# Optimization experiments

Measured on AMD Instinct MI355X. Metric: run time of the kernel, lower is better.

Reference implementation:

```python
import jax, jax.numpy as jnp
import numpy as np

SPIKE_COUNT = 3   # init kwarg spike_count
DT = 0.001        # init kwarg dt; convert_indices_to_times=True


def setup_inputs() -> dict:
    key = jax.random.key(0)
    T, B, N = 512, 64, 2048
    spike_input = jax.random.bernoulli(key, 0.05, (T, B, N)).astype(jnp.float32)
    return {"spike_input": spike_input}


def reference(spike_input):
    """Return times of the first SPIKE_COUNT spikes along the time axis for
    each (batch, output) channel, ascending; channels with fewer spikes are
    padded with inf. Matches norse ToSpikeTimes followed by * dt.
    Input: [T, B, N] -> output: [SPIKE_COUNT, B, N]."""
    T = spike_input.shape[0]
    t_idx = jnp.arange(T, dtype=spike_input.dtype)[:, None, None]        # [T,1,1]
    masked = jnp.where(spike_input > 0, t_idx, jnp.inf)                  # [T,B,N]
    # smallest SPIKE_COUNT indices per channel via top_k on the negation
    neg = -jnp.moveaxis(masked, 0, -1)                                   # [B,N,T]
    vals, _ = jax.lax.top_k(neg, SPIKE_COUNT)                            # [B,N,k]
    spike_idx = jnp.moveaxis(-vals, -1, 0)                               # [k,B,N], ascending
    return spike_idx * DT
```

## Files before the change

kernel.cpp:

```cpp
#include <hip/hip_runtime.h>
#include <cmath>


constexpr int K_SPIKES = 3;
constexpr int CHUNK = 16;

__global__ __launch_bounds__(256) void spikes_to_times_kernel(
    const float* __restrict__ in, float* __restrict__ out,
    int BN, int T, float dt) {
  const int c = blockIdx.x * blockDim.x + threadIdx.x;
  if (c >= BN) return;

  float t0 = INFINITY, t1 = INFINITY, t2 = INFINITY;
  int cnt = 0;
  const float* p = in + c;

  for (int t = 0; t < T; t += CHUNK) {
    float v[CHUNK];
#pragma unroll
    for (int j = 0; j < CHUNK; ++j) {
      v[j] = p[(size_t)(t + j) * (size_t)BN];
    }
#pragma unroll
    for (int j = 0; j < CHUNK; ++j) {
      const bool s = v[j] > 0.0f;
      const float tt = (float)(t + j);
      if (s && cnt == 0) t0 = tt;
      if (s && cnt == 1) t1 = tt;
      if (s && cnt == 2) t2 = tt;
      cnt += s ? 1 : 0;
    }
    if (__all(cnt >= K_SPIKES)) break;
  }

  out[c]          = t0 * dt;
  out[BN + c]     = t1 * dt;
  out[2 * BN + c] = t2 * dt;
}

extern "C" void kernel_launch(void* const* d_in, const int* in_sizes, int n_in,
                              void* d_out, int out_size, void* d_ws, size_t ws_size,
                              hipStream_t stream) {
  const float* in = (const float*)d_in[0];
  float* out = (float*)d_out;

  const int BN = out_size / K_SPIKES;
  const int T = in_sizes[0] / BN;

  const int block = 256;
  const int grid = (BN + block - 1) / block;
  hipLaunchKernelGGL(spikes_to_times_kernel, dim3(grid), dim3(block), 0, stream,
                     in, out, BN, T, 0.001f);
}
```

Measured before the change: 26.99 us.

## Software-pipeline chunk loads with four rotating register buffers

Result: slower. 35.45 us (+31.3%).

```diff
diff --git a/kernel.cpp b/kernel.cpp
--- a/kernel.cpp
+++ b/kernel.cpp
@@ -11,27 +11,61 @@
   const int c = blockIdx.x * blockDim.x + threadIdx.x;
   if (c >= BN) return;
 
+  const int nchunks = (T + CHUNK - 1) / CHUNK;
+  const float* p = in + c;
+
   float t0 = INFINITY, t1 = INFINITY, t2 = INFINITY;
   int cnt = 0;
-  const float* p = in + c;
 
-  for (int t = 0; t < T; t += CHUNK) {
-    float v[CHUNK];
-#pragma unroll
-    for (int j = 0; j < CHUNK; ++j) {
-      v[j] = p[(size_t)(t + j) * (size_t)BN];
-    }
-#pragma unroll
-    for (int j = 0; j < CHUNK; ++j) {
-      const bool s = v[j] > 0.0f;
-      const float tt = (float)(t + j);
-      if (s && cnt == 0) t0 = tt;
-      if (s && cnt == 1) t1 = tt;
-      if (s && cnt == 2) t2 = tt;
-      cnt += s ? 1 : 0;
-    }
+  float b0[CHUNK], b1[CHUNK], b2[CHUNK], b3[CHUNK];
+
+#define LOADC(dst, ci)                                                   \
+  do {                                                                   \
+    const int cc_ = ((ci) < nchunks) ? (ci) : (nchunks - 1);             \
+    _Pragma("unroll") for (int j = 0; j < CHUNK; ++j) {                  \
+      dst[j] = p[(size_t)(cc_ * CHUNK + j) * (size_t)BN];                \
+    }                                                                    \
+  } while (0)
+
+#define PROC(src, ci)                                                    \
+  do {                                                                   \
+    if ((ci) < nchunks) {                                                \
+      _Pragma("unroll") for (int j = 0; j < CHUNK; ++j) {                \
+        const int ti_ = (ci) * CHUNK + j;                                \
+        const bool s_ = (src[j] > 0.0f) && (ti_ < T);                    \
+        const float tt_ = (float)ti_;                                    \
+        if (s_ && cnt == 0) t0 = tt_;                                    \
+        if (s_ && cnt == 1) t1 = tt_;                                    \
+        if (s_ && cnt == 2) t2 = tt_;                                    \
+        cnt += s_ ? 1 : 0;                                               \
+      }                                                                  \
+    }                                                                    \
+  } while (0)
+
+  LOADC(b0, 0);
+  LOADC(b1, 1);
+  LOADC(b2, 2);
+
+  for (int base = 0; base < nchunks; base += 4) {
+    LOADC(b3, base + 3);
+    PROC(b0, base + 0);
+    if (__all(cnt >= K_SPIKES)) break;
+
+    LOADC(b0, base + 4);
+    PROC(b1, base + 1);
+    if (__all(cnt >= K_SPIKES)) break;
+
+    LOADC(b1, base + 5);
+    PROC(b2, base + 2);
+    if (__all(cnt >= K_SPIKES)) break;
+
+    LOADC(b2, base + 6);
+    PROC(b3, base + 3);
     if (__all(cnt >= K_SPIKES)) break;
   }
+
+#undef LOADC
+#undef PROC
 
   out[c]          = t0 * dt;
   out[BN + c]     = t1 * dt;
```

## Vectorize channel loads as float4 and software-pipeline chunk loads with four-stage ring buffer

Applied to the files above, without the earlier changes.

Result: slower. 70.75 us (+162.1%).

```diff
diff --git a/kernel.cpp b/kernel.cpp
--- a/kernel.cpp
+++ b/kernel.cpp
@@ -3,39 +3,90 @@
 
 
 constexpr int K_SPIKES = 3;
-constexpr int CHUNK = 16;
+constexpr int CPT = 4;
+constexpr int CHUNK = 4;
 
-__global__ __launch_bounds__(256) void spikes_to_times_kernel(
+__global__ __launch_bounds__(128) void spikes_to_times_kernel(
     const float* __restrict__ in, float* __restrict__ out,
     int BN, int T, float dt) {
-  const int c = blockIdx.x * blockDim.x + threadIdx.x;
-  if (c >= BN) return;
+  const int tid = blockIdx.x * blockDim.x + threadIdx.x;
+  const int c4 = tid * CPT;
+  if (c4 >= BN) return;
 
-  float t0 = INFINITY, t1 = INFINITY, t2 = INFINITY;
-  int cnt = 0;
-  const float* p = in + c;
+  const int nchunks = (T + CHUNK - 1) / CHUNK;
 
-  for (int t = 0; t < T; t += CHUNK) {
-    float v[CHUNK];
+  float t0[CPT], t1[CPT], t2[CPT];
+  int cnt[CPT];
 #pragma unroll
-    for (int j = 0; j < CHUNK; ++j) {
-      v[j] = p[(size_t)(t + j) * (size_t)BN];
-    }
-#pragma unroll
-    for (int j = 0; j < CHUNK; ++j) {
-      const bool s = v[j] > 0.0f;
-      const float tt = (float)(t + j);
-      if (s && cnt == 0) t0 = tt;
-      if (s && cnt == 1) t1 = tt;
-      if (s && cnt == 2) t2 = tt;
-      cnt += s ? 1 : 0;
-    }
-    if (__all(cnt >= K_SPIKES)) break;
+  for (int k = 0; k < CPT; ++k) {
+    t0[k] = INFINITY; t1[k] = INFINITY; t2[k] = INFINITY; cnt[k] = 0;
   }
 
-  out[c]          = t0 * dt;
-  out[BN + c]     = t1 * dt;
-  out[2 * BN + c] = t2 * dt;
+  float4 bA[CHUNK], bB[CHUNK], bC[CHUNK], bD[CHUNK];
+
+#define LOADC(dst, ci)                                                     \
+  do {                                                                     \
+    const int cc_ = ((ci) < nchunks) ? (ci) : (nchunks - 1);               \
+    _Pragma("unroll") for (int j = 0; j < CHUNK; ++j) {                    \
+      dst[j] = *reinterpret_cast<const float4*>(                           \
+          in + (size_t)(cc_ * CHUNK + j) * (size_t)BN + c4);               \
+    }                                                                      \
+  } while (0)
+
+#define PROC(src, ci)                                                      \
+  do {                                                                     \
+    if ((ci) < nchunks) {                                                  \
+      _Pragma("unroll") for (int j = 0; j < CHUNK; ++j) {                  \
+        const int ti_ = (ci) * CHUNK + j;                                  \
+        const float tt_ = (float)ti_;                                      \
+        const float v_[CPT] = {src[j].x, src[j].y, src[j].z, src[j].w};    \
+        _Pragma("unroll") for (int k = 0; k < CPT; ++k) {                  \
+          const bool s_ = (v_[k] > 0.0f) && (ti_ < T);                     \
+          if (s_ && cnt[k] == 0) t0[k] = tt_;                              \
+          if (s_ && cnt[k] == 1) t1[k] = tt_;                              \
+          if (s_ && cnt[k] == 2) t2[k] = tt_;                              \
+          cnt[k] += s_ ? 1 : 0;                                            \
+        }                                                                  \
+      }                                                                    \
+    }                                                                      \
+  } while (0)
+
+#define DONE()                                                             \
+  (cnt[0] >= K_SPIKES && cnt[1] >= K_SPIKES && cnt[2] >= K_SPIKES &&       \
+   cnt[3] >= K_SPIKES)
+
+  LOADC(bA, 0);
+  LOADC(bB, 1);
+  LOADC(bC, 2);
+
+  for (int base = 0; base < nchunks; base += 4) {
+    LOADC(bD, base + 3);
+    PROC(bA, base + 0);
+    if (__all(DONE())) break;
+
+    LOADC(bA, base + 4);
+    PROC(bB, base + 1);
+    if (__all(DONE())) break;
+
+    LOADC(bB, base + 5);
+    PROC(bC, base + 2);
+    if (__all(DONE())) break;
+
+    LOADC(bC, base + 6);
+    PROC(bD, base + 3);
+    if (__all(DONE())) break;
+  }
+
+#undef LOADC
+#undef PROC
+#undef DONE
+
+  const float4 o0 = make_float4(t0[0] * dt, t0[1] * dt, t0[2] * dt, t0[3] * dt);
+  const float4 o1 = make_float4(t1[0] * dt, t1[1] * dt, t1[2] * dt, t1[3] * dt);
+  const float4 o2 = make_float4(t2[0] * dt, t2[1] * dt, t2[2] * dt, t2[3] * dt);
+  *reinterpret_cast<float4*>(out + c4) = o0;
+  *reinterpret_cast<float4*>(out + BN + c4) = o1;
+  *reinterpret_cast<float4*>(out + 2 * (size_t)BN + c4) = o2;
 }
 
 extern "C" void kernel_launch(void* const* d_in, const int* in_sizes, int n_in,
@@ -47,8 +98,9 @@
   const int BN = out_size / K_SPIKES;
   const int T = in_sizes[0] / BN;
 
-  const int block = 256;
-  const int grid = (BN + block - 1) / block;
+  const int threads = BN / CPT;
+  const int block = 128;
+  const int grid = (threads + block - 1) / block;
   hipLaunchKernelGGL(spikes_to_times_kernel, dim3(grid), dim3(block), 0, stream,
                      in, out, BN, T, 0.001f);
 }
```

## Stage spike rows through double-buffered LDS with float4 loads and block-wide early exit

Applied to the files above, without the earlier changes.

Result: slower. 64.42 us (+138.7%).

```diff
diff --git a/kernel.cpp b/kernel.cpp
--- a/kernel.cpp
+++ b/kernel.cpp
@@ -3,39 +3,95 @@
 
 
 constexpr int K_SPIKES = 3;
-constexpr int CHUNK = 16;
+constexpr int BLOCK_CH = 256;
+constexpr int GROUP = 16;
+constexpr int ROWS_PER_WAVE = 4;
 
-__global__ __launch_bounds__(256) void spikes_to_times_kernel(
+__global__ __launch_bounds__(BLOCK_CH) void spikes_to_times_kernel(
     const float* __restrict__ in, float* __restrict__ out,
     int BN, int T, float dt) {
-  const int c = blockIdx.x * blockDim.x + threadIdx.x;
-  if (c >= BN) return;
+  __shared__ float4 lds4[2][GROUP][BLOCK_CH / 4];
+  const float* ldsF = reinterpret_cast<const float*>(&lds4[0][0][0]);
+
+  const int tidx = threadIdx.x;
+  const int wave = tidx >> 6;
+  const int lane = tidx & 63;
+  const int c0 = blockIdx.x * BLOCK_CH;
+  const int c = c0 + tidx;
+  const int ngroups = (T + GROUP - 1) / GROUP;
+
+  int c4 = c0 + 4 * lane;
+  if (c4 > BN - 4) c4 = BN - 4;
 
   float t0 = INFINITY, t1 = INFINITY, t2 = INFINITY;
   int cnt = 0;
-  const float* p = in + c;
 
-  for (int t = 0; t < T; t += CHUNK) {
-    float v[CHUNK];
-#pragma unroll
-    for (int j = 0; j < CHUNK; ++j) {
-      v[j] = p[(size_t)(t + j) * (size_t)BN];
-    }
-#pragma unroll
-    for (int j = 0; j < CHUNK; ++j) {
-      const bool s = v[j] > 0.0f;
-      const float tt = (float)(t + j);
-      if (s && cnt == 0) t0 = tt;
-      if (s && cnt == 1) t1 = tt;
-      if (s && cnt == 2) t2 = tt;
-      cnt += s ? 1 : 0;
-    }
-    if (__all(cnt >= K_SPIKES)) break;
+  struct RowRegs { float4 r0, r1, r2, r3; };
+  RowRegs rA, rB;
+
+#define LD(row)                                                          \
+  (*reinterpret_cast<const float4*>(                                     \
+      in + (size_t)(((row) < T) ? (row) : (T - 1)) * (size_t)BN + c4))
+
+#define LOADG(dst, gi)                                                   \
+  do {                                                                   \
+    const int gg_ = ((gi) < ngroups) ? (gi) : (ngroups - 1);             \
+    const int rb_ = gg_ * GROUP + wave;                                  \
+    dst.r0 = LD(rb_);                                                    \
+    dst.r1 = LD(rb_ + 4);                                                \
+    dst.r2 = LD(rb_ + 8);                                                \
+    dst.r3 = LD(rb_ + 12);                                               \
+  } while (0)
+
+#define WRITEG(src, bf)                                                  \
+  do {                                                                   \
+    lds4[bf][wave][lane] = src.r0;                                       \
+    lds4[bf][wave + 4][lane] = src.r1;                                   \
+    lds4[bf][wave + 8][lane] = src.r2;                                   \
+    lds4[bf][wave + 12][lane] = src.r3;                                  \
+  } while (0)
+
+#define SCANG(bf, gi)                                                    \
+  do {                                                                   \
+    _Pragma("unroll") for (int r_ = 0; r_ < GROUP; ++r_) {               \
+      const int ti_ = (gi)*GROUP + r_;                                   \
+      const float v_ = ldsF[((bf)*GROUP + r_) * BLOCK_CH + tidx];        \
+      const bool s_ = (v_ > 0.0f) && (ti_ < T);                          \
+      const float tt_ = (float)ti_;                                      \
+      if (s_ && cnt == 0) t0 = tt_;                                      \
+      if (s_ && cnt == 1) t1 = tt_;                                      \
+      if (s_ && cnt == 2) t2 = tt_;                                      \
+      cnt += s_ ? 1 : 0;                                                 \
+    }                                                                    \
+  } while (0)
+
+  LOADG(rA, 0);
+  LOADG(rB, 1);
+  WRITEG(rA, 0);
+  __syncthreads();
+
+  for (int g = 0; g < ngroups; g += 2) {
+    LOADG(rA, g + 2);
+    WRITEG(rB, 1);
+    SCANG(0, g);
+    if (__syncthreads_and((cnt >= K_SPIKES) || (c >= BN))) break;
+
+    LOADG(rB, g + 3);
+    WRITEG(rA, 0);
+    SCANG(1, g + 1);
+    if (__syncthreads_and((cnt >= K_SPIKES) || (c >= BN))) break;
   }
 
-  out[c]          = t0 * dt;
-  out[BN + c]     = t1 * dt;
-  out[2 * BN + c] = t2 * dt;
+#undef LD
+#undef LOADG
+#undef WRITEG
+#undef SCANG
+
+  if (c < BN) {
+    out[c] = t0 * dt;
+    out[BN + c] = t1 * dt;
+    out[2 * (size_t)BN + c] = t2 * dt;
+  }
 }
 
 extern "C" void kernel_launch(void* const* d_in, const int* in_sizes, int n_in,
@@ -47,8 +103,7 @@
   const int BN = out_size / K_SPIKES;
   const int T = in_sizes[0] / BN;
 
-  const int block = 256;
-  const int grid = (BN + block - 1) / block;
-  hipLaunchKernelGGL(spikes_to_times_kernel, dim3(grid), dim3(block), 0, stream,
-                     in, out, BN, T, 0.001f);
+  const int grid = (BN + BLOCK_CH - 1) / BLOCK_CH;
+  hipLaunchKernelGGL(spikes_to_times_kernel, dim3(grid), dim3(BLOCK_CH), 0,
+                     stream, in, out, BN, T, 0.001f);
 }
```
